# Optimization experiments

Measured on AMD Instinct MI355X. Metric: run time of the kernel, lower is better.

## Reference

```python
import jax, jax.numpy as jnp
import numpy as np

L, B, S, D = 12, 2, 2048, 768
QK, H, V = 128, 512, 32000
SCALE = 128 ** (-0.5)


def setup_inputs() -> dict:
    key = jax.random.key(0)
    ks = jax.random.split(key, 11)
    p = lambda k, shp: jax.random.normal(k, shp, dtype=jnp.float32) * 0.02
    return {
        "layer_outputs": jax.random.normal(ks[0], (L, B, S, D), dtype=jnp.float32),
        "Wq": p(ks[1], (D, QK)), "bq": jnp.zeros((QK,), jnp.float32),
        "Wk": p(ks[2], (D, QK)), "bk": jnp.zeros((QK,), jnp.float32),
        "Wv": p(ks[3], (D, H)),  "bv": jnp.zeros((H,), jnp.float32),
        "W1": p(ks[4], (H, H // 2)), "b1": jnp.zeros((H // 2,), jnp.float32),
        "W2": p(ks[5], (H // 2, V)), "b2": jnp.zeros((V,), jnp.float32),
    }


def reference(layer_outputs, Wq, bq, Wk, bk, Wv, bv, W1, b1, W2, b2):
    # layer_outputs: (L, B, S, D) -> h: (S, L, B, D) as in torch permute(2,0,1,3)
    h = jnp.transpose(layer_outputs, (2, 0, 1, 3))
    q_in = h.mean(axis=1)                              # (S, B, D)
    q = jax.nn.relu(q_in @ Wq + bq)                    # (S, B, 128)
    k = jax.nn.relu(h @ Wk + bk)                       # (S, L, B, 128)
    scores = jnp.einsum('sbd,slbd->slb', q, k)[..., None] * SCALE  # (S, L, B, 1)
    attn = jax.nn.softmax(scores, axis=1)              # softmax over layer axis
    v = h @ Wv + bv                                    # (S, L, B, H)
    agg = jnp.sum(attn * v, axis=1)                    # (S, B, H)
    agg = jnp.transpose(agg, (1, 0, 2))                # (B, S, H)
    mid = jax.nn.relu(agg @ W1 + b1)                   # (B, S, H//2); dropout is eval-mode identity
    return mid @ W2 + b2                               # (B, S, V)
```

## Files before the change

### kernel.cpp

```cpp
#include <hip/hip_runtime.h>

#define Snum 2048
#define SCALE 0.08838834764831845f

typedef __attribute__((ext_vector_type(8))) __bf16 bf16x8;
typedef __attribute__((ext_vector_type(4))) float f32x4;

__device__ inline unsigned short f2bf(float f) {
    unsigned int u = __float_as_uint(f);
    unsigned int r = u + 0x7FFFu + ((u >> 16) & 1u);
    return (unsigned short)(r >> 16);
}
__device__ inline float bf2f(unsigned short u) {
    return __uint_as_float(((unsigned)u) << 16);
}
__device__ inline void gld_lds16(const unsigned short* g, unsigned short* l) {
    __builtin_amdgcn_global_load_lds(
        (const __attribute__((address_space(1))) unsigned int*)g,
        (__attribute__((address_space(3))) unsigned int*)l, 16, 0, 0);
}

__global__ __launch_bounds__(256) void transpose_f2bf(
    const float* __restrict__ in, unsigned short* __restrict__ out, int K, int N)
{
    __shared__ float t[32][33];
    const int bx = blockIdx.x;
    const int by = blockIdx.y;
    const int tx = threadIdx.x & 31, ty = threadIdx.x >> 5;
    #pragma unroll
    for (int i = 0; i < 4; ++i) {
        int k = by * 32 + ty + i * 8, n = bx * 32 + tx;
        t[ty + i * 8][tx] = in[(size_t)k * N + n];
    }
    __syncthreads();
    #pragma unroll
    for (int i = 0; i < 4; ++i) {
        int n = bx * 32 + ty + i * 8, k = by * 32 + tx;
        out[(size_t)n * K + k] = f2bf(t[tx][ty + i * 8]);
    }
}

__global__ __launch_bounds__(512) void proj_qk(
    const float* __restrict__ x, const unsigned short* __restrict__ Bt,
    const float* __restrict__ bk,
    unsigned short* __restrict__ Kall,
    unsigned short* __restrict__ Pq)
{
    __shared__ __align__(16) unsigned short As[128 * 32];
    __shared__ __align__(16) unsigned short Bs[256 * 32];
    const int tid = threadIdx.x;
    const int wid = tid >> 6, lane = tid & 63;
    const int wm = (wid >> 2) * 64, wn = (wid & 3) * 64;
    const int lr = lane & 15, g = lane >> 4;
    const int r0 = blockIdx.x * 128;
    const int K = 768;

    f32x4 acc[4][4] = {};
    const int arow = tid >> 2, akc = (tid & 2) * 4;
    const int arow2 = tid >> 2, akc2 = (tid & 3) * 8;
    (void)arow; (void)akc;

    for (int k0 = 0; k0 < K; k0 += 32) {
        __syncthreads();
        {
            const float* src = x + (size_t)(r0 + arow2) * K + k0 + akc2;
            float4 v0 = *(const float4*)src;
            float4 v1 = *(const float4*)(src + 4);
            unsigned short v[8];
            v[0] = f2bf(v0.x); v[1] = f2bf(v0.y); v[2] = f2bf(v0.z); v[3] = f2bf(v0.w);
            v[4] = f2bf(v1.x); v[5] = f2bf(v1.y); v[6] = f2bf(v1.z); v[7] = f2bf(v1.w);
            *(uint4*)&As[arow2 * 32 + akc2] = *(uint4*)v;
        }
        #pragma unroll
        for (int c = 0; c < 2; ++c) {
            int rr = wid * 32 + c * 16;
            gld_lds16(Bt + (size_t)(rr + (lane >> 2)) * K + k0 + (lane & 3) * 8,
                      &Bs[rr * 32]);
        }
        __syncthreads();

        bf16x8 aF[4], bF[4];
        #pragma unroll
        for (int mm = 0; mm < 4; ++mm) aF[mm] = *(const bf16x8*)&As[(wm + mm * 16 + lr) * 32 + g * 8];
        #pragma unroll
        for (int nn = 0; nn < 4; ++nn) bF[nn] = *(const bf16x8*)&Bs[(wn + nn * 16 + lr) * 32 + g * 8];
        #pragma unroll
        for (int mm = 0; mm < 4; ++mm)
            #pragma unroll
            for (int nn = 0; nn < 4; ++nn)
                acc[mm][nn] = __builtin_amdgcn_mfma_f32_16x16x32_bf16(aF[mm], bF[nn], acc[mm][nn], 0, 0, 0);
    }

    #pragma unroll
    for (int mm = 0; mm < 4; ++mm)
        #pragma unroll
        for (int nn = 0; nn < 4; ++nn) {
            int col = wn + nn * 16 + lr;
            #pragma unroll
            for (int reg = 0; reg < 4; ++reg) {
                int orow = r0 + wm + mm * 16 + g * 4 + reg;
                float v = acc[mm][nn][reg];
                if (col < 128) {
                    float kv = v + bk[col];
                    Kall[(size_t)orow * 128 + col] = f2bf(kv > 0.f ? kv : 0.f);
                } else {
                    Pq[(size_t)orow * 128 + (col - 128)] = f2bf(v);
                }
            }
        }
}

__global__ __launch_bounds__(256) void qreduce(
    const unsigned short* __restrict__ Pq, const float* __restrict__ bq,
    unsigned short* __restrict__ Q)
{
    const int t = blockIdx.x * 256 + threadIdx.x;
    const int r = t >> 4, jg = t & 15;
    const int b = r >> 11, s = r & 2047;
    float acc[8] = {};
    #pragma unroll
    for (int l = 0; l < 12; ++l) {
        const unsigned short* src = Pq + ((size_t)(l * 2 + b) * Snum + s) * 128 + jg * 8;
        uint4 u = *(const uint4*)src;
        const unsigned short* v = (const unsigned short*)&u;
        #pragma unroll
        for (int i = 0; i < 8; ++i) acc[i] += bf2f(v[i]);
    }
    unsigned short o[8];
    #pragma unroll
    for (int i = 0; i < 8; ++i) {
        float q = acc[i] * (1.0f / 12.0f) + bq[jg * 8 + i];
        o[i] = f2bf(q > 0.f ? q : 0.f);
    }
    *(uint4*)(Q + (size_t)r * 128 + jg * 8) = *(uint4*)o;
}

__global__ __launch_bounds__(256) void scores_hbar(
    const float* __restrict__ x,
    const unsigned short* __restrict__ Q,
    const unsigned short* __restrict__ Kall,
    unsigned short* __restrict__ hbar)
{
    const int wid = threadIdx.x >> 6, lane = threadIdx.x & 63;
    const int r = blockIdx.x * 4 + wid;
    const int b = r >> 11, s = r & 2047;

    const unsigned short* qrow = Q + (size_t)r * 128 + lane * 2;
    const float q0 = bf2f(qrow[0]), q1 = bf2f(qrow[1]);

    float sc[12];
    #pragma unroll
    for (int l = 0; l < 12; ++l) {
        const unsigned short* krow = Kall + ((size_t)(l * 2 + b) * Snum + s) * 128 + lane * 2;
        float p = q0 * bf2f(krow[0]) + q1 * bf2f(krow[1]);
        #pragma unroll
        for (int off = 32; off > 0; off >>= 1) p += __shfl_xor(p, off, 64);
        sc[l] = p * SCALE;
    }
    float m = sc[0];
    #pragma unroll
    for (int l = 1; l < 12; ++l) m = fmaxf(m, sc[l]);
    float att[12], den = 0.f;
    #pragma unroll
    for (int l = 0; l < 12; ++l) { att[l] = __expf(sc[l] - m); den += att[l]; }
    const float inv = 1.0f / den;
    #pragma unroll
    for (int l = 0; l < 12; ++l) att[l] *= inv;

    #pragma unroll
    for (int jv = 0; jv < 3; ++jv) {
        const int d0 = jv * 256 + lane * 4;
        float a0 = 0.f, a1 = 0.f, a2 = 0.f, a3 = 0.f;
        #pragma unroll
        for (int l = 0; l < 12; ++l) {
            const float4 v = *(const float4*)(x + ((size_t)(l * 2 + b) * Snum + s) * 768 + d0);
            a0 += att[l] * v.x; a1 += att[l] * v.y; a2 += att[l] * v.z; a3 += att[l] * v.w;
        }
        ushort4 o;
        o.x = f2bf(a0); o.y = f2bf(a1); o.z = f2bf(a2); o.w = f2bf(a3);
        *(ushort4*)(hbar + (size_t)r * 768 + d0) = o;
    }
}

template <int RELU, int OUT_BF16>
__global__ __launch_bounds__(256) void gemm64(
    const unsigned short* __restrict__ A, const unsigned short* __restrict__ Bt,
    const float* __restrict__ bias, void* __restrict__ out, int M, int N, int K)
{
    __shared__ __align__(16) unsigned short As[64][40];
    __shared__ __align__(16) unsigned short Bs[64][40];
    const int tid = threadIdx.x;
    const int bn = blockIdx.x, bm = blockIdx.y;
    const int wid = tid >> 6, lane = tid & 63;
    const int wm = (wid >> 1) * 32, wn = (wid & 1) * 32;
    const int lr = lane & 15, g = lane >> 4;
    const int r0 = bm * 64, c0 = bn * 64;

    f32x4 acc[2][2] = {};
    const int row = tid >> 2, kc = (tid & 3) * 8;

    for (int k0 = 0; k0 < K; k0 += 32) {
        __syncthreads();
        *(uint4*)&As[row][kc] = *(const uint4*)(A  + (size_t)(r0 + row) * K + k0 + kc);
        *(uint4*)&Bs[row][kc] = *(const uint4*)(Bt + (size_t)(c0 + row) * K + k0 + kc);
        __syncthreads();

        bf16x8 aF[2], bF[2];
        #pragma unroll
        for (int mm = 0; mm < 2; ++mm) aF[mm] = *(const bf16x8*)&As[wm + mm * 16 + lr][g * 8];
        #pragma unroll
        for (int nn = 0; nn < 2; ++nn) bF[nn] = *(const bf16x8*)&Bs[wn + nn * 16 + lr][g * 8];
        #pragma unroll
        for (int mm = 0; mm < 2; ++mm)
            #pragma unroll
            for (int nn = 0; nn < 2; ++nn)
                acc[mm][nn] = __builtin_amdgcn_mfma_f32_16x16x32_bf16(aF[mm], bF[nn], acc[mm][nn], 0, 0, 0);
    }

    #pragma unroll
    for (int mm = 0; mm < 2; ++mm)
        #pragma unroll
        for (int nn = 0; nn < 2; ++nn) {
            int col = c0 + wn + nn * 16 + lr;
            float bcol = bias[col];
            #pragma unroll
            for (int reg = 0; reg < 4; ++reg) {
                int orow = r0 + wm + mm * 16 + g * 4 + reg;
                float v = acc[mm][nn][reg] + bcol;
                if (RELU) v = v > 0.f ? v : 0.f;
                if (OUT_BF16) ((unsigned short*)out)[(size_t)orow * N + col] = f2bf(v);
                else          ((float*)out)[(size_t)orow * N + col] = v;
            }
        }
}

__global__ __launch_bounds__(256) void gemm_out(
    const unsigned short* __restrict__ A,
    const unsigned short* __restrict__ Bt,
    const float* __restrict__ bias, float* __restrict__ out)
{
    __shared__ __align__(16) unsigned short As[128 * 32];
    __shared__ __align__(16) unsigned short Bs[128 * 32];
    const int K = 256, N = 32000;
    const int orig = blockIdx.x;
    const int swz = (orig & 7) * 1000 + (orig >> 3);
    const int bn = swz >> 5;
    const int bm = swz & 31;
    const int tid = threadIdx.x;
    const int wid = tid >> 6, lane = tid & 63;
    const int wm = (wid >> 1) * 64, wn = (wid & 1) * 64;
    const int lr = lane & 15, g = lane >> 4;
    const int r0 = bm * 128, c0 = bn * 128;

    f32x4 acc[4][4] = {};

    for (int k0 = 0; k0 < K; k0 += 32) {
        __syncthreads();
        #pragma unroll
        for (int c = 0; c < 2; ++c) {
            int rr = wid * 32 + c * 16;
            gld_lds16(A  + (size_t)(r0 + rr + (lane >> 2)) * K + k0 + (lane & 3) * 8, &As[rr * 32]);
            gld_lds16(Bt + (size_t)(c0 + rr + (lane >> 2)) * K + k0 + (lane & 3) * 8, &Bs[rr * 32]);
        }
        __syncthreads();

        bf16x8 aF[4], bF[4];
        #pragma unroll
        for (int mm = 0; mm < 4; ++mm) aF[mm] = *(const bf16x8*)&As[(wm + mm * 16 + lr) * 32 + g * 8];
        #pragma unroll
        for (int nn = 0; nn < 4; ++nn) bF[nn] = *(const bf16x8*)&Bs[(wn + nn * 16 + lr) * 32 + g * 8];
        #pragma unroll
        for (int mm = 0; mm < 4; ++mm)
            #pragma unroll
            for (int nn = 0; nn < 4; ++nn)
                acc[mm][nn] = __builtin_amdgcn_mfma_f32_16x16x32_bf16(aF[mm], bF[nn], acc[mm][nn], 0, 0, 0);
    }

    #pragma unroll
    for (int mm = 0; mm < 4; ++mm)
        #pragma unroll
        for (int nn = 0; nn < 4; ++nn) {
            int col = c0 + wn + nn * 16 + lr;
            float bcol = bias[col];
            #pragma unroll
            for (int reg = 0; reg < 4; ++reg) {
                int orow = r0 + wm + mm * 16 + g * 4 + reg;
                out[(size_t)orow * N + col] = acc[mm][nn][reg] + bcol;
            }
        }
}

extern "C" void kernel_launch(void* const* d_in, const int* in_sizes, int n_in,
                              void* d_out, int out_size, void* d_ws, size_t ws_size,
                              hipStream_t stream) {
    (void)in_sizes; (void)n_in; (void)out_size; (void)ws_size;

    const float* x  = (const float*)d_in[0];
    const float* Wq = (const float*)d_in[1];
    const float* bq = (const float*)d_in[2];
    const float* Wk = (const float*)d_in[3];
    const float* bk = (const float*)d_in[4];
    const float* Wv = (const float*)d_in[5];
    const float* bv = (const float*)d_in[6];
    const float* W1 = (const float*)d_in[7];
    const float* b1 = (const float*)d_in[8];
    const float* W2 = (const float*)d_in[9];
    const float* b2 = (const float*)d_in[10];

    char* p = (char*)d_ws;
    unsigned short* Wqkt  = (unsigned short*)p; p += (size_t)256 * 768 * 2;
    unsigned short* Wvt   = (unsigned short*)p; p += (size_t)512 * 768 * 2;
    unsigned short* W1t   = (unsigned short*)p; p += (size_t)256 * 512 * 2;
    unsigned short* W2t   = (unsigned short*)p; p += (size_t)32000 * 256 * 2;
    unsigned short* Qb    = (unsigned short*)p; p += (size_t)4096 * 128 * 2;
    unsigned short* Kall  = (unsigned short*)p; p += (size_t)49152 * 128 * 2;
    unsigned short* Pq    = (unsigned short*)p; p += (size_t)49152 * 128 * 2;
    unsigned short* hbar  = (unsigned short*)p; p += (size_t)4096 * 768 * 2;
    unsigned short* aggb  = (unsigned short*)p; p += (size_t)4096 * 512 * 2;
    unsigned short* midb  = (unsigned short*)p; p += (size_t)4096 * 256 * 2;

    transpose_f2bf<<<dim3(128 / 32, 768 / 32), dim3(256), 0, stream>>>(Wk, Wqkt, 768, 128);
    transpose_f2bf<<<dim3(128 / 32, 768 / 32), dim3(256), 0, stream>>>(Wq, Wqkt + (size_t)128 * 768, 768, 128);
    transpose_f2bf<<<dim3(512 / 32, 768 / 32), dim3(256), 0, stream>>>(Wv, Wvt, 768, 512);
    transpose_f2bf<<<dim3(256 / 32, 512 / 32), dim3(256), 0, stream>>>(W1, W1t, 512, 256);
    transpose_f2bf<<<dim3(32000 / 32, 256 / 32), dim3(256), 0, stream>>>(W2, W2t, 256, 32000);

    proj_qk<<<dim3(49152 / 128), dim3(512), 0, stream>>>(x, Wqkt, bk, Kall, Pq);

    qreduce<<<dim3(4096 * 16 / 256), dim3(256), 0, stream>>>(Pq, bq, Qb);

    scores_hbar<<<dim3(1024), dim3(256), 0, stream>>>(x, Qb, Kall, hbar);

    gemm64<0, 1><<<dim3(512 / 64, 4096 / 64), dim3(256), 0, stream>>>(
        hbar, Wvt, bv, aggb, 4096, 512, 768);

    gemm64<1, 1><<<dim3(256 / 64, 4096 / 64), dim3(256), 0, stream>>>(
        aggb, W1t, b1, midb, 4096, 256, 512);

    gemm_out<<<dim3(8000), dim3(256), 0, stream>>>(midb, W2t, b2, (float*)d_out);
}
```

Before: 340.8 us.

## Double-buffer proj_qk and gemm_out LDS tiles, fold qreduce into scores kernel

Adds LDS double buffering to proj_qk and gemm_out so global loads for the next K-tile are issued before the MFMAs on the current tile, with one barrier per iteration. proj_qk is also reshaped to 64-row tiles with 256 threads, giving twice as many blocks. The separate qreduce kernel is removed: scores_hbar now averages the Pq rows itself and applies bias and relu, saving a launch and the Q round trip through memory. The cost is more LDS per block and some redundant Pq reads inside the scores kernel.

```diff
diff --git a/kernel.cpp b/kernel.cpp
--- a/kernel.cpp
+++ b/kernel.cpp
@@ -40,55 +40,72 @@
     }
 }
 
-__global__ __launch_bounds__(512) void proj_qk(
+__global__ __launch_bounds__(256) void proj_qk(
     const float* __restrict__ x, const unsigned short* __restrict__ Bt,
     const float* __restrict__ bk,
     unsigned short* __restrict__ Kall,
     unsigned short* __restrict__ Pq)
 {
-    __shared__ __align__(16) unsigned short As[128 * 32];
-    __shared__ __align__(16) unsigned short Bs[256 * 32];
+    __shared__ __align__(16) unsigned short As[2][64 * 32];
+    __shared__ __align__(16) unsigned short Bs[2][256 * 32];
     const int tid = threadIdx.x;
     const int wid = tid >> 6, lane = tid & 63;
-    const int wm = (wid >> 2) * 64, wn = (wid & 3) * 64;
+    const int wn = wid * 64;
     const int lr = lane & 15, g = lane >> 4;
-    const int r0 = blockIdx.x * 128;
-    const int K = 768;
+    const int r0 = blockIdx.x * 64;
+    const int K = 768, NT = K / 32;
+
+    const int arow = tid >> 2, akc = (tid & 3) * 8;
 
     f32x4 acc[4][4] = {};
-    const int arow = tid >> 2, akc = (tid & 2) * 4;
-    const int arow2 = tid >> 2, akc2 = (tid & 3) * 8;
-    (void)arow; (void)akc;
-
-    for (int k0 = 0; k0 < K; k0 += 32) {
-        __syncthreads();
-        {
-            const float* src = x + (size_t)(r0 + arow2) * K + k0 + akc2;
-            float4 v0 = *(const float4*)src;
-            float4 v1 = *(const float4*)(src + 4);
-            unsigned short v[8];
-            v[0] = f2bf(v0.x); v[1] = f2bf(v0.y); v[2] = f2bf(v0.z); v[3] = f2bf(v0.w);
-            v[4] = f2bf(v1.x); v[5] = f2bf(v1.y); v[6] = f2bf(v1.z); v[7] = f2bf(v1.w);
-            *(uint4*)&As[arow2 * 32 + akc2] = *(uint4*)v;
-        }
-        #pragma unroll
-        for (int c = 0; c < 2; ++c) {
-            int rr = wid * 32 + c * 16;
-            gld_lds16(Bt + (size_t)(rr + (lane >> 2)) * K + k0 + (lane & 3) * 8,
-                      &Bs[rr * 32]);
-        }
-        __syncthreads();
+
+    float4 a0 = *(const float4*)(x + (size_t)(r0 + arow) * K + akc);
+    float4 a1 = *(const float4*)(x + (size_t)(r0 + arow) * K + akc + 4);
+    {
+        unsigned short v[8];
+        v[0] = f2bf(a0.x); v[1] = f2bf(a0.y); v[2] = f2bf(a0.z); v[3] = f2bf(a0.w);
+        v[4] = f2bf(a1.x); v[5] = f2bf(a1.y); v[6] = f2bf(a1.z); v[7] = f2bf(a1.w);
+        *(uint4*)&As[0][arow * 32 + akc] = *(uint4*)v;
+    }
+    #pragma unroll
+    for (int c = 0; c < 4; ++c) {
+        int rr = wid * 64 + c * 16;
+        gld_lds16(Bt + (size_t)(rr + (lane >> 2)) * K + (lane & 3) * 8, &Bs[0][rr * 32]);
+    }
+    __syncthreads();
+
+    for (int t = 0; t < NT; ++t) {
+        const int cur = t & 1, nxt = cur ^ 1;
+        if (t + 1 < NT) {
+            const int k0 = (t + 1) * 32;
+            a0 = *(const float4*)(x + (size_t)(r0 + arow) * K + k0 + akc);
+            a1 = *(const float4*)(x + (size_t)(r0 + arow) * K + k0 + akc + 4);
+            #pragma unroll
+            for (int c = 0; c < 4; ++c) {
+                int rr = wid * 64 + c * 16;
+                gld_lds16(Bt + (size_t)(rr + (lane >> 2)) * K + k0 + (lane & 3) * 8,
+                          &Bs[nxt][rr * 32]);
+            }
+        }
 
         bf16x8 aF[4], bF[4];
         #pragma unroll
-        for (int mm = 0; mm < 4; ++mm) aF[mm] = *(const bf16x8*)&As[(wm + mm * 16 + lr) * 32 + g * 8];
-        #pragma unroll
-        for (int nn = 0; nn < 4; ++nn) bF[nn] = *(const bf16x8*)&Bs[(wn + nn * 16 + lr) * 32 + g * 8];
+        for (int mm = 0; mm < 4; ++mm) aF[mm] = *(const bf16x8*)&As[cur][(mm * 16 + lr) * 32 + g * 8];
+        #pragma unroll
+        for (int nn = 0; nn < 4; ++nn) bF[nn] = *(const bf16x8*)&Bs[cur][(wn + nn * 16 + lr) * 32 + g * 8];
         #pragma unroll
         for (int mm = 0; mm < 4; ++mm)
             #pragma unroll
             for (int nn = 0; nn < 4; ++nn)
                 acc[mm][nn] = __builtin_amdgcn_mfma_f32_16x16x32_bf16(aF[mm], bF[nn], acc[mm][nn], 0, 0, 0);
+
+        if (t + 1 < NT) {
+            unsigned short v[8];
+            v[0] = f2bf(a0.x); v[1] = f2bf(a0.y); v[2] = f2bf(a0.z); v[3] = f2bf(a0.w);
+            v[4] = f2bf(a1.x); v[5] = f2bf(a1.y); v[6] = f2bf(a1.z); v[7] = f2bf(a1.w);
+            *(uint4*)&As[nxt][arow * 32 + akc] = *(uint4*)v;
+        }
+        __syncthreads();
     }
 
     #pragma unroll
@@ -98,7 +115,7 @@
             int col = wn + nn * 16 + lr;
             #pragma unroll
             for (int reg = 0; reg < 4; ++reg) {
-                int orow = r0 + wm + mm * 16 + g * 4 + reg;
+                int orow = r0 + mm * 16 + g * 4 + reg;
                 float v = acc[mm][nn][reg];
                 if (col < 128) {
                     float kv = v + bk[col];
@@ -110,34 +127,10 @@
         }
 }
 
-__global__ __launch_bounds__(256) void qreduce(
-    const unsigned short* __restrict__ Pq, const float* __restrict__ bq,
-    unsigned short* __restrict__ Q)
-{
-    const int t = blockIdx.x * 256 + threadIdx.x;
-    const int r = t >> 4, jg = t & 15;
-    const int b = r >> 11, s = r & 2047;
-    float acc[8] = {};
-    #pragma unroll
-    for (int l = 0; l < 12; ++l) {
-        const unsigned short* src = Pq + ((size_t)(l * 2 + b) * Snum + s) * 128 + jg * 8;
-        uint4 u = *(const uint4*)src;
-        const unsigned short* v = (const unsigned short*)&u;
-        #pragma unroll
-        for (int i = 0; i < 8; ++i) acc[i] += bf2f(v[i]);
-    }
-    unsigned short o[8];
-    #pragma unroll
-    for (int i = 0; i < 8; ++i) {
-        float q = acc[i] * (1.0f / 12.0f) + bq[jg * 8 + i];
-        o[i] = f2bf(q > 0.f ? q : 0.f);
-    }
-    *(uint4*)(Q + (size_t)r * 128 + jg * 8) = *(uint4*)o;
-}
-
 __global__ __launch_bounds__(256) void scores_hbar(
     const float* __restrict__ x,
-    const unsigned short* __restrict__ Q,
+    const unsigned short* __restrict__ Pq,
+    const float* __restrict__ bq,
     const unsigned short* __restrict__ Kall,
     unsigned short* __restrict__ hbar)
 {
@@ -145,14 +138,26 @@
     const int r = blockIdx.x * 4 + wid;
     const int b = r >> 11, s = r & 2047;
 
-    const unsigned short* qrow = Q + (size_t)r * 128 + lane * 2;
-    const float q0 = bf2f(qrow[0]), q1 = bf2f(qrow[1]);
+    float qa = 0.f, qb_ = 0.f;
+    #pragma unroll
+    for (int l = 0; l < 12; ++l) {
+        const unsigned short* prow = Pq + ((size_t)(l * 2 + b) * Snum + s) * 128 + lane * 2;
+        unsigned int u = *(const unsigned int*)prow;
+        qa += bf2f((unsigned short)(u & 0xFFFF));
+        qb_ += bf2f((unsigned short)(u >> 16));
+    }
+    float q0 = qa * (1.0f / 12.0f) + bq[lane * 2];
+    float q1 = qb_ * (1.0f / 12.0f) + bq[lane * 2 + 1];
+    q0 = q0 > 0.f ? q0 : 0.f;
+    q1 = q1 > 0.f ? q1 : 0.f;
+    q0 = bf2f(f2bf(q0)); q1 = bf2f(f2bf(q1));
 
     float sc[12];
     #pragma unroll
     for (int l = 0; l < 12; ++l) {
         const unsigned short* krow = Kall + ((size_t)(l * 2 + b) * Snum + s) * 128 + lane * 2;
-        float p = q0 * bf2f(krow[0]) + q1 * bf2f(krow[1]);
+        unsigned int u = *(const unsigned int*)krow;
+        float p = q0 * bf2f((unsigned short)(u & 0xFFFF)) + q1 * bf2f((unsigned short)(u >> 16));
         #pragma unroll
         for (int off = 32; off > 0; off >>= 1) p += __shfl_xor(p, off, 64);
         sc[l] = p * SCALE;
@@ -239,9 +244,9 @@
     const unsigned short* __restrict__ Bt,
     const float* __restrict__ bias, float* __restrict__ out)
 {
-    __shared__ __align__(16) unsigned short As[128 * 32];
-    __shared__ __align__(16) unsigned short Bs[128 * 32];
-    const int K = 256, N = 32000;
+    __shared__ __align__(16) unsigned short As[2][128 * 32];
+    __shared__ __align__(16) unsigned short Bs[2][128 * 32];
+    const int K = 256, N = 32000, NT = K / 32;
     const int orig = blockIdx.x;
     const int swz = (orig & 7) * 1000 + (orig >> 3);
     const int bn = swz >> 5;
@@ -254,26 +259,37 @@
 
     f32x4 acc[4][4] = {};
 
-    for (int k0 = 0; k0 < K; k0 += 32) {
-        __syncthreads();
-        #pragma unroll
-        for (int c = 0; c < 2; ++c) {
-            int rr = wid * 32 + c * 16;
-            gld_lds16(A  + (size_t)(r0 + rr + (lane >> 2)) * K + k0 + (lane & 3) * 8, &As[rr * 32]);
-            gld_lds16(Bt + (size_t)(c0 + rr + (lane >> 2)) * K + k0 + (lane & 3) * 8, &Bs[rr * 32]);
-        }
-        __syncthreads();
+    #pragma unroll
+    for (int c = 0; c < 2; ++c) {
+        int rr = wid * 32 + c * 16;
+        gld_lds16(A  + (size_t)(r0 + rr + (lane >> 2)) * K + (lane & 3) * 8, &As[0][rr * 32]);
+        gld_lds16(Bt + (size_t)(c0 + rr + (lane >> 2)) * K + (lane & 3) * 8, &Bs[0][rr * 32]);
+    }
+    __syncthreads();
+
+    for (int t = 0; t < NT; ++t) {
+        const int cur = t & 1, nxt = cur ^ 1;
+        if (t + 1 < NT) {
+            const int k0 = (t + 1) * 32;
+            #pragma unroll
+            for (int c = 0; c < 2; ++c) {
+                int rr = wid * 32 + c * 16;
+                gld_lds16(A  + (size_t)(r0 + rr + (lane >> 2)) * K + k0 + (lane & 3) * 8, &As[nxt][rr * 32]);
+                gld_lds16(Bt + (size_t)(c0 + rr + (lane >> 2)) * K + k0 + (lane & 3) * 8, &Bs[nxt][rr * 32]);
+            }
+        }
 
         bf16x8 aF[4], bF[4];
         #pragma unroll
-        for (int mm = 0; mm < 4; ++mm) aF[mm] = *(const bf16x8*)&As[(wm + mm * 16 + lr) * 32 + g * 8];
-        #pragma unroll
-        for (int nn = 0; nn < 4; ++nn) bF[nn] = *(const bf16x8*)&Bs[(wn + nn * 16 + lr) * 32 + g * 8];
+        for (int mm = 0; mm < 4; ++mm) aF[mm] = *(const bf16x8*)&As[cur][(wm + mm * 16 + lr) * 32 + g * 8];
+        #pragma unroll
+        for (int nn = 0; nn < 4; ++nn) bF[nn] = *(const bf16x8*)&Bs[cur][(wn + nn * 16 + lr) * 32 + g * 8];
         #pragma unroll
         for (int mm = 0; mm < 4; ++mm)
             #pragma unroll
             for (int nn = 0; nn < 4; ++nn)
                 acc[mm][nn] = __builtin_amdgcn_mfma_f32_16x16x32_bf16(aF[mm], bF[nn], acc[mm][nn], 0, 0, 0);
+        __syncthreads();
     }
 
     #pragma unroll
@@ -312,7 +328,6 @@
     unsigned short* Wvt   = (unsigned short*)p; p += (size_t)512 * 768 * 2;
     unsigned short* W1t   = (unsigned short*)p; p += (size_t)256 * 512 * 2;
     unsigned short* W2t   = (unsigned short*)p; p += (size_t)32000 * 256 * 2;
-    unsigned short* Qb    = (unsigned short*)p; p += (size_t)4096 * 128 * 2;
     unsigned short* Kall  = (unsigned short*)p; p += (size_t)49152 * 128 * 2;
     unsigned short* Pq    = (unsigned short*)p; p += (size_t)49152 * 128 * 2;
     unsigned short* hbar  = (unsigned short*)p; p += (size_t)4096 * 768 * 2;
@@ -325,11 +340,9 @@
     transpose_f2bf<<<dim3(256 / 32, 512 / 32), dim3(256), 0, stream>>>(W1, W1t, 512, 256);
     transpose_f2bf<<<dim3(32000 / 32, 256 / 32), dim3(256), 0, stream>>>(W2, W2t, 256, 32000);
 
-    proj_qk<<<dim3(49152 / 128), dim3(512), 0, stream>>>(x, Wqkt, bk, Kall, Pq);
-
-    qreduce<<<dim3(4096 * 16 / 256), dim3(256), 0, stream>>>(Pq, bq, Qb);
-
-    scores_hbar<<<dim3(1024), dim3(256), 0, stream>>>(x, Qb, Kall, hbar);
+    proj_qk<<<dim3(49152 / 64), dim3(256), 0, stream>>>(x, Wqkt, bk, Kall, Pq);
+
+    scores_hbar<<<dim3(1024), dim3(256), 0, stream>>>(x, Pq, bq, Kall, hbar);
 
     gemm64<0, 1><<<dim3(512 / 64, 4096 / 64), dim3(256), 0, stream>>>(
         hbar, Wvt, bv, aggb, 4096, 512, 768);
```

Result: no change. 340.2 us (-0.2%).
